# Kernel optimization log

Measured on AMD Instinct MI355X. Metric: run time of the kernel, lower is better.

The kernel has to match this reference:

```python
import jax, jax.numpy as jnp
import numpy as np

B = 65536
NC = 64          # coarse samples
NF = 128         # fine samples
NEAR, FAR = 2.0, 6.0


def setup_inputs() -> dict:
    key = jax.random.key(0)
    k1, k2, k3, k4, k5, k6 = jax.random.split(key, 6)
    ray_origin = jax.random.normal(k1, (B, 3), dtype=jnp.float32)
    ray_direction = jax.random.normal(k2, (B, 3), dtype=jnp.float32)
    # stratified linspace depths, as in the coarse branch of _sample_points_on_ray
    step = (FAR - NEAR) / (NC - 1)
    coarse_depth_values = jnp.broadcast_to(
        NEAR + jnp.arange(NC, dtype=jnp.float32) * step, (B, NC)
    )
    coarse_weights = jax.random.uniform(k3, (B, NC), dtype=jnp.float32)
    u = jax.random.uniform(k4, (B, NF), dtype=jnp.float32)
    raw_density = jax.random.uniform(k5, (B, NC + NF, 1), dtype=jnp.float32)
    raw_color = jax.random.uniform(k6, (B, NC + NF, 3), dtype=jnp.float32)
    return {
        "ray_origin": ray_origin,
        "ray_direction": ray_direction,
        "coarse_depth_values": coarse_depth_values,
        "coarse_weights": coarse_weights,
        "u": u,
        "raw_density": raw_density,
        "raw_color": raw_color,
    }


def _sample_pdf(bins, weights, u):
    """Inverse-CDF sampling. bins: [B, M+1], weights: [B, M], u: [B, N]."""
    M = weights.shape[1]
    weights = weights + 1e-5
    pdf = weights / jnp.sum(weights, axis=-1, keepdims=True)
    cdf = jnp.cumsum(pdf, axis=-1)                     # [B, M]
    cdf = jnp.concatenate([jnp.zeros_like(cdf[:, :1]), cdf], axis=-1)  # [B, M+1]
    # torch loop `above_inds += (u >= cdf[:, i])` for i in [0, M) ==
    # searchsorted(cdf[:, :M], u, side='right')
    above = jax.vmap(lambda c, uu: jnp.searchsorted(c, uu, side="right"))(
        cdf[:, :M], u
    )                                                  # [B, N], values in [1, M]
    below = jnp.clip(above - 1, 0, None)
    cdf_b = jnp.take_along_axis(cdf, below, axis=-1)
    cdf_a = jnp.take_along_axis(cdf, above, axis=-1)
    bins_b = jnp.take_along_axis(bins, below, axis=-1)
    bins_a = jnp.take_along_axis(bins, above, axis=-1)
    denom = cdf_a - cdf_b
    denom = jnp.where(denom < 1e-5, jnp.ones_like(denom), denom)
    t = (u - cdf_b) / denom
    return bins_b + t * (bins_a - bins_b)


def _composite(raw_density, raw_color, depth_values):
    # distances between consecutive samples, last one = 1e10
    dists = depth_values[..., 1:] - depth_values[..., :-1]
    dists = jnp.concatenate(
        [dists, jnp.full_like(dists[:, :1], 1e10)], axis=-1
    )
    alpha = 1.0 - jnp.exp(-raw_density[..., 0] * dists)          # [B, S]
    T = jnp.cumprod(1.0 - alpha + 1e-10, axis=-1)[:, :-1]
    T = jnp.concatenate([jnp.ones_like(T[:, :1]), T], axis=-1)
    weights = T * alpha                                           # [B, S]
    depth = jnp.sum(weights * depth_values, axis=-1, keepdims=True)
    color = jnp.sum(weights[..., None] * raw_color, axis=-2)      # [B, 3]
    return depth, color, weights


def reference(ray_origin, ray_direction, coarse_depth_values, coarse_weights,
              u, raw_density, raw_color):
    # fine branch of _sample_points_on_ray
    mids = 0.5 * (coarse_depth_values[..., 1:] + coarse_depth_values[..., :-1])
    w = coarse_weights[:, 1:-1]
    fine_depths = _sample_pdf(mids, w, u)                         # [B, NF]
    depth_values = jnp.sort(
        jnp.concatenate([coarse_depth_values, fine_depths], axis=-1), axis=-1
    )                                                             # [B, NC+NF]
    points_on_ray = (
        ray_origin[:, None, :]
        + ray_direction[:, None, :] * depth_values[..., None]
    )                                                             # [B, S, 3]
    depth, color_map, weights = _composite(raw_density, raw_color, depth_values)
    # forward of RenderRay returns the color map; points kept live via dummy use
    del points_on_ray, depth, weights
    return color_map
```

## Files before the change

### kernel.cpp

```cpp
#include <hip/hip_runtime.h>

#define NC 64
#define NF 128
#define NT 192
#define B_TOTAL 65536
#define RPB 4

#define NEAR_F 2.0f
#define STEP_F (4.0f / 63.0f)

template<int CTRL, int RM>
__device__ __forceinline__ float updpp_f(float oldv, float v) {
    return __int_as_float(__builtin_amdgcn_update_dpp(
        __float_as_int(oldv), __float_as_int(v), CTRL, RM, 0xf, false));
}
template<int CTRL, int RM>
__device__ __forceinline__ int updpp_i(int oldv, int v) {
    return __builtin_amdgcn_update_dpp(oldv, v, CTRL, RM, 0xf, false);
}

__device__ __forceinline__ float wave_iscan_add_f(float v) {
    v += updpp_f<0x111, 0xf>(0.0f, v);
    v += updpp_f<0x112, 0xf>(0.0f, v);
    v += updpp_f<0x114, 0xf>(0.0f, v);
    v += updpp_f<0x118, 0xf>(0.0f, v);
    v += updpp_f<0x142, 0xa>(0.0f, v);
    v += updpp_f<0x143, 0xc>(0.0f, v);
    return v;
}
__device__ __forceinline__ float wave_iscan_mul_f(float v) {
    v *= updpp_f<0x111, 0xf>(1.0f, v);
    v *= updpp_f<0x112, 0xf>(1.0f, v);
    v *= updpp_f<0x114, 0xf>(1.0f, v);
    v *= updpp_f<0x118, 0xf>(1.0f, v);
    v *= updpp_f<0x142, 0xa>(1.0f, v);
    v *= updpp_f<0x143, 0xc>(1.0f, v);
    return v;
}
__device__ __forceinline__ int wave_iscan_add_i(int v) {
    v += updpp_i<0x111, 0xf>(0, v);
    v += updpp_i<0x112, 0xf>(0, v);
    v += updpp_i<0x114, 0xf>(0, v);
    v += updpp_i<0x118, 0xf>(0, v);
    v += updpp_i<0x142, 0xa>(0, v);
    v += updpp_i<0x143, 0xc>(0, v);
    return v;
}

__device__ __forceinline__ void wave_fence() {
    __builtin_amdgcn_wave_barrier();
    __asm__ volatile("" ::: "memory");
}

__global__ __launch_bounds__(256) void render_ray_kernel(
    const float* __restrict__ cw,
    const float* __restrict__ u_in,
    const float* __restrict__ dens,
    const float* __restrict__ col,
    float* __restrict__ out)
{
    const int wave = threadIdx.x >> 6;
    const int lane = threadIdx.x & 63;
    const int ray  = blockIdx.x * RPB + wave;

    __shared__ float s_cdf [RPB][64];
    __shared__ float s_m   [RPB][200];
    __shared__ int   s_hist[RPB][64];

    const float wraw = cw[(size_t)ray * NC + lane];
    float x = u_in[(size_t)ray * NF + lane];
    float y = u_in[(size_t)ray * NF + 64 + lane];

    const float wv = (lane >= 1 && lane <= 62) ? (wraw + 1e-5f) : 0.0f;
    float ssum = wv;
    #pragma unroll
    for (int off = 32; off; off >>= 1) ssum += __shfl_xor(ssum, off);
    const float pdf = __fdividef(wv, ssum);
    s_cdf[wave][lane]  = wave_iscan_add_f(pdf);
    s_hist[wave][lane] = 0;
    wave_fence();

    #pragma unroll
    for (int k = 2; k <= 128; k <<= 1) {
        #pragma unroll
        for (int j = k >> 1; j > 0; j >>= 1) {
            if (j == 64) {
                const float mn = fminf(x, y);
                const float mx = fmaxf(x, y);
                x = mn; y = mx;
            } else {
                const bool up = (lane & j) != 0;
                const bool dx = (lane & k) != 0;
                const bool dy = ((lane + 64) & k) != 0;
                const float px = __shfl_xor(x, j);
                const float py = __shfl_xor(y, j);
                const bool cx = x < px;
                const bool cy = y < py;
                x = ((cx != up) != dx) ? x : px;
                y = ((cy != up) != dy) ? y : py;
            }
        }
    }

    const float* __restrict__ cdfp = s_cdf[wave];
    auto sample = [&](float u, int& g) -> float {
        int l = 0;
        #pragma unroll
        for (int s = 32; s; s >>= 1) {
            const int t = l + s;
            if (cdfp[t - 1] <= u) l = t;
        }
        l = min(l, 62);
        const int below = l - 1;
        const float cb = cdfp[below];
        const float ca = cdfp[l];
        float denom = ca - cb;
        if (denom < 1e-5f) denom = 1.0f;
        const float t = __fdividef(u - cb, denom);
        g = below + 1 + ((t >= 0.5f) ? 1 : 0);
        return NEAR_F + ((float)below + 0.5f + t) * STEP_F;
    };

    int gx, gy;
    const float fx = sample(x, gx);
    const float fy = sample(y, gy);

    s_m[wave][lane + gx]      = fx;
    s_m[wave][lane + 64 + gy] = fy;
    atomicAdd(&s_hist[wave][gx], 1);
    atomicAdd(&s_hist[wave][gy], 1);
    wave_fence();

    const int hsum = wave_iscan_add_i(s_hist[wave][lane]);
    s_m[wave][lane + hsum] = NEAR_F + (float)lane * STEP_F;
    wave_fence();

    const float* __restrict__ mp = s_m[wave];
    const int i0 = 3 * lane;
    const float m0 = mp[i0], m1 = mp[i0 + 1], m2 = mp[i0 + 2];
    const float m3 = mp[i0 + 3];
    const float d0 = m1 - m0;
    const float d1 = m2 - m1;
    const float d2 = (lane == 63) ? 1e10f : (m3 - m2);

    const float* __restrict__ dp = dens + (size_t)ray * NT + i0;
    const float a0 = 1.0f - __expf(-dp[0] * d0);
    const float a1 = 1.0f - __expf(-dp[1] * d1);
    const float a2 = 1.0f - __expf(-dp[2] * d2);
    const float f0 = 1.0f - a0 + 1e-10f;
    const float f1 = 1.0f - a1 + 1e-10f;
    const float f2 = 1.0f - a2 + 1e-10f;

    float scanp = wave_iscan_mul_f(f0 * f1 * f2);
    float T0 = __shfl_up(scanp, 1);
    if (lane == 0) T0 = 1.0f;
    const float T1 = T0 * f0;
    const float T2 = T1 * f1;

    const float w0 = T0 * (1.0f - f0 + 1e-10f);
    const float w1 = T1 * (1.0f - f1 + 1e-10f);
    const float w2 = T2 * (1.0f - f2 + 1e-10f);

    const float* __restrict__ cp = col + (size_t)ray * NT * 3 + 3 * (size_t)i0;
    float ax = w0 * cp[0] + w1 * cp[3] + w2 * cp[6];
    float ay = w0 * cp[1] + w1 * cp[4] + w2 * cp[7];
    float az = w0 * cp[2] + w1 * cp[5] + w2 * cp[8];

    #pragma unroll
    for (int off = 32; off; off >>= 1) {
        ax += __shfl_xor(ax, off);
        ay += __shfl_xor(ay, off);
        az += __shfl_xor(az, off);
    }
    if (lane == 0) {
        out[(size_t)ray * 3 + 0] = ax;
        out[(size_t)ray * 3 + 1] = ay;
        out[(size_t)ray * 3 + 2] = az;
    }
}

extern "C" void kernel_launch(void* const* d_in, const int* in_sizes, int n_in,
                              void* d_out, int out_size, void* d_ws, size_t ws_size,
                              hipStream_t stream) {
    const float* cwts = (const float*)d_in[3];
    const float* u    = (const float*)d_in[4];
    const float* dens = (const float*)d_in[5];
    const float* col  = (const float*)d_in[6];
    float* out = (float*)d_out;

    dim3 grid(B_TOTAL / RPB);
    dim3 block(256);
    hipLaunchKernelGGL(render_ray_kernel, grid, block, 0, stream,
                       cwts, u, dens, col, out);
}
```

Measured before the change: 291.3 us.

## Prefetch density/color early and replace shuffles with DPP scans and readlane search

Loads of density and color are issued at kernel start so their latency overlaps the CDF build, sort and sampling. The pdf normalization reduction becomes a single scan plus readlane, and the first three binary-search levels use wave-uniform readlane values instead of LDS reads. The exclusive transmittance is computed by dividing by the lane's own product instead of a shfl_up, and the final color reductions use DPP scans. The bin index g is now derived from the sample depth via floor, which may change rounding at bin boundaries, and the division-based transmittance can lose precision or produce NaN when the product underflows.

```diff
diff --git a/kernel.cpp b/kernel.cpp
--- a/kernel.cpp
+++ b/kernel.cpp
@@ -8,6 +8,7 @@
 
 #define NEAR_F 2.0f
 #define STEP_F (4.0f / 63.0f)
+#define INV_STEP (63.0f / 4.0f)
 
 template<int CTRL, int RM>
 __device__ __forceinline__ float updpp_f(float oldv, float v) {
@@ -45,6 +46,10 @@
     v += updpp_i<0x142, 0xa>(0, v);
     v += updpp_i<0x143, 0xc>(0, v);
     return v;
+}
+
+__device__ __forceinline__ float rlane_f(float v, int l) {
+    return __int_as_float(__builtin_amdgcn_readlane(__float_as_int(v), l));
 }
 
 __device__ __forceinline__ void wave_fence() {
@@ -71,13 +76,25 @@
     float x = u_in[(size_t)ray * NF + lane];
     float y = u_in[(size_t)ray * NF + 64 + lane];
 
+    const int i0 = 3 * lane;
+    const float* __restrict__ dp = dens + (size_t)ray * NT + i0;
+    const float dv0 = dp[0], dv1 = dp[1], dv2 = dp[2];
+    const float* __restrict__ cp = col + ((size_t)ray * NT + (size_t)i0) * 3;
+    float cc[9];
+    #pragma unroll
+    for (int q = 0; q < 9; ++q) cc[q] = cp[q];
+
     const float wv = (lane >= 1 && lane <= 62) ? (wraw + 1e-5f) : 0.0f;
-    float ssum = wv;
-    #pragma unroll
-    for (int off = 32; off; off >>= 1) ssum += __shfl_xor(ssum, off);
-    const float pdf = __fdividef(wv, ssum);
-    s_cdf[wave][lane]  = wave_iscan_add_f(pdf);
+    const float sc = wave_iscan_add_f(wv);
+    const float total = rlane_f(sc, 63);
+    const float cdfv = __fdividef(sc, total);
+    s_cdf[wave][lane]  = cdfv;
     s_hist[wave][lane] = 0;
+
+    const float c31 = rlane_f(cdfv, 31);
+    const float c15 = rlane_f(cdfv, 15), c47 = rlane_f(cdfv, 47);
+    const float c7  = rlane_f(cdfv, 7),  c23 = rlane_f(cdfv, 23);
+    const float c39 = rlane_f(cdfv, 39), c55 = rlane_f(cdfv, 55);
     wave_fence();
 
     #pragma unroll
@@ -104,12 +121,16 @@
 
     const float* __restrict__ cdfp = s_cdf[wave];
     auto sample = [&](float u, int& g) -> float {
-        int l = 0;
-        #pragma unroll
-        for (int s = 32; s; s >>= 1) {
-            const int t = l + s;
-            if (cdfp[t - 1] <= u) l = t;
-        }
+        int l = (c31 <= u) ? 32 : 0;
+        const float p16 = (l == 0) ? c15 : c47;
+        if (p16 <= u) l += 16;
+        const float pa = ((l & 16) == 0) ? c7  : c23;
+        const float pb = ((l & 16) == 0) ? c39 : c55;
+        const float p8 = ((l & 32) == 0) ? pa : pb;
+        if (p8 <= u) l += 8;
+        if (cdfp[l + 3] <= u) l += 4;
+        if (cdfp[l + 1] <= u) l += 2;
+        if (cdfp[l]     <= u) l += 1;
         l = min(l, 62);
         const int below = l - 1;
         const float cb = cdfp[below];
@@ -117,8 +138,10 @@
         float denom = ca - cb;
         if (denom < 1e-5f) denom = 1.0f;
         const float t = __fdividef(u - cb, denom);
-        g = below + 1 + ((t >= 0.5f) ? 1 : 0);
-        return NEAR_F + ((float)below + 0.5f + t) * STEP_F;
+        const float f = NEAR_F + ((float)below + 0.5f + t) * STEP_F;
+        int gi = (int)floorf((f - NEAR_F) * INV_STEP) + 1;
+        g = min(max(gi, 1), 63);
+        return f;
     };
 
     int gx, gy;
@@ -136,24 +159,22 @@
     wave_fence();
 
     const float* __restrict__ mp = s_m[wave];
-    const int i0 = 3 * lane;
     const float m0 = mp[i0], m1 = mp[i0 + 1], m2 = mp[i0 + 2];
     const float m3 = mp[i0 + 3];
     const float d0 = m1 - m0;
     const float d1 = m2 - m1;
     const float d2 = (lane == 63) ? 1e10f : (m3 - m2);
 
-    const float* __restrict__ dp = dens + (size_t)ray * NT + i0;
-    const float a0 = 1.0f - __expf(-dp[0] * d0);
-    const float a1 = 1.0f - __expf(-dp[1] * d1);
-    const float a2 = 1.0f - __expf(-dp[2] * d2);
+    const float a0 = 1.0f - __expf(-dv0 * d0);
+    const float a1 = 1.0f - __expf(-dv1 * d1);
+    const float a2 = 1.0f - __expf(-dv2 * d2);
     const float f0 = 1.0f - a0 + 1e-10f;
     const float f1 = 1.0f - a1 + 1e-10f;
     const float f2 = 1.0f - a2 + 1e-10f;
 
-    float scanp = wave_iscan_mul_f(f0 * f1 * f2);
-    float T0 = __shfl_up(scanp, 1);
-    if (lane == 0) T0 = 1.0f;
+    const float prod  = f0 * f1 * f2;
+    const float scanp = wave_iscan_mul_f(prod);
+    const float T0 = __fdividef(scanp, prod);
     const float T1 = T0 * f0;
     const float T2 = T1 * f1;
 
@@ -161,18 +182,14 @@
     const float w1 = T1 * (1.0f - f1 + 1e-10f);
     const float w2 = T2 * (1.0f - f2 + 1e-10f);
 
-    const float* __restrict__ cp = col + (size_t)ray * NT * 3 + 3 * (size_t)i0;
-    float ax = w0 * cp[0] + w1 * cp[3] + w2 * cp[6];
-    float ay = w0 * cp[1] + w1 * cp[4] + w2 * cp[7];
-    float az = w0 * cp[2] + w1 * cp[5] + w2 * cp[8];
-
-    #pragma unroll
-    for (int off = 32; off; off >>= 1) {
-        ax += __shfl_xor(ax, off);
-        ay += __shfl_xor(ay, off);
-        az += __shfl_xor(az, off);
-    }
-    if (lane == 0) {
+    float ax = w0 * cc[0] + w1 * cc[3] + w2 * cc[6];
+    float ay = w0 * cc[1] + w1 * cc[4] + w2 * cc[7];
+    float az = w0 * cc[2] + w1 * cc[5] + w2 * cc[8];
+
+    ax = wave_iscan_add_f(ax);
+    ay = wave_iscan_add_f(ay);
+    az = wave_iscan_add_f(az);
+    if (lane == 63) {
         out[(size_t)ray * 3 + 0] = ax;
         out[(size_t)ray * 3 + 1] = ay;
         out[(size_t)ray * 3 + 2] = az;
```

Result: no change. 288.1 us (-1.1%).
